# Kernel optimization log

Measured on AMD Instinct MI355X. Metric: run time of the kernel, lower is better.

The kernel has to match this reference:

```python
import jax, jax.numpy as jnp
import numpy as np

B, E, H, W = 32, 512, 16, 16
NH, HD = 8, 64          # num_heads = embed_dim // num_heads_channels, head_dim = 64
OUT = 512
S = H * W + 1           # spacial_dim**2 + 1 = 257 (mean token prepended)


def setup_inputs() -> dict:
    key = jax.random.key(0)
    ks = jax.random.split(key, 10)
    sc = 1.0 / np.sqrt(E).astype(np.float32)
    n = lambda k, sh, s=1.0: jax.random.normal(k, sh, jnp.float32) * s
    return {
        "x_real": n(ks[0], (B, E, H, W)),
        "x_imag": n(ks[1], (B, E, H, W)),
        # positional_embedding = (randn/sqrt(E)).to(complex64) -> imag part is zero
        "pos_r": n(ks[2], (E, S), sc),
        "pos_i": jnp.zeros((E, S), jnp.float32),
        # complex in-projection (packed q,k,v) and out-projection of the MHA
        "w_in_r": n(ks[3], (3 * E, E), sc),
        "w_in_i": n(ks[4], (3 * E, E), sc),
        "b_in_r": jnp.zeros((3 * E,), jnp.float32),
        "b_in_i": jnp.zeros((3 * E,), jnp.float32),
        "w_out_r": n(ks[5], (E, E), sc),
        "w_out_i": n(ks[6], (E, E), sc),
        "b_out_r": jnp.zeros((E,), jnp.float32),
        "b_out_i": jnp.zeros((E,), jnp.float32),
        # complex 1x1 conv projection == complex linear over channels
        "w_p_r": n(ks[7], (OUT, E), sc),
        "w_p_i": n(ks[8], (OUT, E), sc),
        "b_p_r": jnp.zeros((OUT,), jnp.float32),
        "b_p_i": jnp.zeros((OUT,), jnp.float32),
    }


def _attention_pool(x_real, x_imag, pos_r, pos_i, w_in_r, w_in_i, b_in_r, b_in_i,
                    w_out_r, w_out_i, b_out_r, b_out_i, w_p_r, w_p_i, b_p_r, b_p_i):
    cx = jax.lax.complex
    x = cx(x_real, x_imag).reshape(B, E, -1)                       # [b,c,HW]
    x = jnp.concatenate([x.mean(-1, keepdims=True), x], axis=-1)   # [b,c,S]
    x = x + cx(pos_r, pos_i)[None]                                 # + pos embed
    x = x.transpose(0, 2, 1)                                       # [b,S,E]

    qkv = jnp.einsum('bse,fe->bsf', x, cx(w_in_r, w_in_i)) + cx(b_in_r, b_in_i)
    q, k, v = jnp.split(qkv, 3, axis=-1)
    q = q.reshape(B, S, NH, HD) / jnp.sqrt(jnp.float32(HD))
    k = k.reshape(B, S, NH, HD)
    v = v.reshape(B, S, NH, HD)

    logits = jnp.einsum('bqhd,bkhd->bhqk', q, k)                   # complex scores
    # complex softmax handled separately on real/imag parts
    w = cx(jax.nn.softmax(logits.real, axis=-1),
           jax.nn.softmax(logits.imag, axis=-1))
    attn = jnp.einsum('bhqk,bkhd->bqhd', w, v).reshape(B, S, E)
    attn = jnp.einsum('bse,fe->bsf', attn, cx(w_out_r, w_out_i)) + cx(b_out_r, b_out_i)

    y = attn.transpose(0, 2, 1)                                    # [b,E,S]
    y = jnp.einsum('oc,bcs->bos', cx(w_p_r, w_p_i), y) + cx(b_p_r, b_p_i)[None, :, None]
    return y[:, :, 0]                                              # [b,OUT] complex64


def reference(x_real, x_imag, pos_r, pos_i, w_in_r, w_in_i, b_in_r, b_in_i,
              w_out_r, w_out_i, b_out_r, b_out_i, w_p_r, w_p_i, b_p_r, b_p_i):
    return _attention_pool(x_real, x_imag, pos_r, pos_i, w_in_r, w_in_i, b_in_r,
                           b_in_i, w_out_r, w_out_i, b_out_r, b_out_i,
                           w_p_r, w_p_i, b_p_r, b_p_i)
```

## Files before the change

### kernel.cpp

```cpp
#include <hip/hip_runtime.h>

#define B_   32
#define E_   512
#define HW_  256
#define S_   257
#define NH_  8
#define NBLK 1024
#define NTHR 256
#define NGRP 32
#define GSZ  32
#define LG_  260

__device__ __forceinline__ void st_sys(float* p, float v) {
  __hip_atomic_store(p, v, __ATOMIC_RELAXED, __HIP_MEMORY_SCOPE_SYSTEM);
}
__device__ __forceinline__ void st_sys2(float2* p, float2 v) {
  unsigned long long u;
  __builtin_memcpy(&u, &v, 8);
  __hip_atomic_store((unsigned long long*)p, u, __ATOMIC_RELAXED, __HIP_MEMORY_SCOPE_SYSTEM);
}

__device__ __forceinline__ float wave_reduce(float v) {
  #pragma unroll
  for (int o = 32; o > 0; o >>= 1) v += __shfl_down(v, o, 64);
  return v;
}

__device__ __forceinline__ void gbar(unsigned* slots, int g, int j, int t, unsigned phase) {
  __syncthreads();
  if (t < 64) {
    if (t == 0)
      __hip_atomic_store(&slots[g * GSZ + j], phase, __ATOMIC_RELAXED, __HIP_MEMORY_SCOPE_SYSTEM);
    const unsigned* line = slots + g * GSZ;
    int sl = t & 31;
    for (;;) {
      unsigned v = __hip_atomic_load(&line[sl], __ATOMIC_RELAXED, __HIP_MEMORY_SCOPE_SYSTEM);
      if (__all((int)(v >= phase))) break;
      __builtin_amdgcn_s_sleep(8);
    }
  }
  __syncthreads();
}

__device__ void softmax257(float* l, float* red, int t) {
  int lane = t & 63, wv = t >> 6;
  float v = l[t];
  float v256 = l[256];
  float m = v;
  #pragma unroll
  for (int o = 32; o > 0; o >>= 1) m = fmaxf(m, __shfl_xor(m, o, 64));
  if (lane == 0) red[wv] = m;
  __syncthreads();
  float M = fmaxf(fmaxf(fmaxf(red[0], red[1]), fmaxf(red[2], red[3])), v256);
  float ex = expf(v - M);
  float e256 = expf(v256 - M);
  float s = ex;
  #pragma unroll
  for (int o = 32; o > 0; o >>= 1) s += __shfl_xor(s, o, 64);
  if (lane == 0) red[4 + wv] = s;
  __syncthreads();
  float inv = 1.f / (red[4] + red[5] + red[6] + red[7] + e256);
  l[t] = ex * inv;
  if (t == 0) l[256] = e256 * inv;
  __syncthreads();
}

__global__ __launch_bounds__(NTHR, 4) void k_mega(
    const float* __restrict__ xr, const float* __restrict__ xi,
    const float* __restrict__ pos_r, const float* __restrict__ pos_i,
    const float* __restrict__ w_in_r, const float* __restrict__ w_in_i,
    const float* __restrict__ b_in_r, const float* __restrict__ b_in_i,
    const float* __restrict__ w_out_r, const float* __restrict__ w_out_i,
    const float* __restrict__ b_out_r, const float* __restrict__ b_out_i,
    const float* __restrict__ w_p_r, const float* __restrict__ w_p_i,
    const float* __restrict__ b_p_r, const float* __restrict__ b_p_i,
    unsigned* slots,
    float* __restrict__ ur_, float* __restrict__ ui_,
    float* __restrict__ lgr, float* __restrict__ lgi,
    float* __restrict__ a0r, float* __restrict__ a0i,
    float* __restrict__ mr, float* __restrict__ mi,
    float* __restrict__ w2,
    float* __restrict__ out, int interleaved) {
  __shared__ __align__(16) float smF[4368];
  const int t   = threadIdx.x;
  const int l   = t & 63;
  const int w   = t >> 6;
  const int bid = blockIdx.x;
  const int g   = bid >> 5;
  const int j   = bid & 31;

  #pragma unroll
  for (int rr = 0; rr < 4; ++rr) {
    int e = j * 16 + w * 4 + rr;
    float4 vr = ((const float4*)(xr + ((size_t)g * E_ + e) * HW_))[l];
    float4 vi = ((const float4*)(xi + ((size_t)g * E_ + e) * HW_))[l];
    float sr = (vr.x + vr.y) + (vr.z + vr.w);
    float si = (vi.x + vi.y) + (vi.z + vi.w);
    sr = wave_reduce(sr); si = wave_reduce(si);
    if (l == 0) {
      st_sys(&mr[g * E_ + e], sr * (1.f / HW_) + pos_r[(size_t)e * S_]);
      st_sys(&mi[g * E_ + e], si * (1.f / HW_) + pos_i[(size_t)e * S_]);
    }
  }
  gbar(slots, g, j, t, 1);

  {
    float* mR  = smF;
    float* mI  = smF + 512;
    float* q0L = smF + 1024;
    mR[t]       = mr[g * E_ + t];        mI[t]       = mi[g * E_ + t];
    mR[t + 256] = mr[g * E_ + t + 256];  mI[t + 256] = mi[g * E_ + t + 256];
    __syncthreads();
    #pragma unroll
    for (int rr = 0; rr < 4; ++rr) {
      int fl = w * 4 + rr;
      int f  = 16 * j + fl;
      const float* wr = w_in_r + (size_t)f * E_;
      const float* wi = w_in_i + (size_t)f * E_;
      float ar = 0.f, ai = 0.f;
      #pragma unroll
      for (int e = l; e < E_; e += 64) {
        float Xr = mR[e], Xi = mI[e], Cr = wr[e], Ci = wi[e];
        ar += Xr * Cr - Xi * Ci;
        ai += Xr * Ci + Xi * Cr;
      }
      ar = wave_reduce(ar); ai = wave_reduce(ai);
      if (l == 0) {
        q0L[fl * 2]     = (ar + b_in_r[f]) * 0.125f;
        q0L[fl * 2 + 1] = (ai + b_in_i[f]) * 0.125f;
      }
    }
    __syncthreads();
    int h = j >> 2;
    float u0r = 0.f, u0i = 0.f, u1r = 0.f, u1i = 0.f;
    #pragma unroll 4
    for (int fl = 0; fl < 16; ++fl) {
      int f = 16 * j + fl;
      float qr = q0L[fl * 2], qi = q0L[fl * 2 + 1];
      const float* Wr = w_in_r + (size_t)(E_ + f) * E_;
      const float* Wi = w_in_i + (size_t)(E_ + f) * E_;
      float W0r = Wr[t], W0i = Wi[t], W1r = Wr[t + 256], W1i = Wi[t + 256];
      u0r += qr * W0r - qi * W0i;  u0i += qr * W0i + qi * W0r;
      u1r += qr * W1r - qi * W1i;  u1i += qr * W1i + qi * W1r;
    }
    size_t ub = (size_t)(g * NH_ + h) * E_;
    atomicAdd(&ur_[ub + t], u0r);        atomicAdd(&ui_[ub + t], u0i);
    atomicAdd(&ur_[ub + t + 256], u1r);  atomicAdd(&ui_[ub + t + 256], u1i);
  }
  gbar(slots, g, j, t, 2);

  {
    int e0 = 16 * j;
    float* us = smF;
    if (t < 128) {
      int e = t & 15, hh = t >> 4;
      us[(e * 8 + hh) * 2]     = ur_[(size_t)(g * NH_ + hh) * E_ + e0 + e];
      us[(e * 8 + hh) * 2 + 1] = ui_[(size_t)(g * NH_ + hh) * E_ + e0 + e];
    }
    __syncthreads();
    float ar[NH_], ai[NH_];
    #pragma unroll
    for (int hh = 0; hh < NH_; ++hh) { ar[hh] = 0.f; ai[hh] = 0.f; }
    const float* xrb = xr + ((size_t)g * E_ + e0) * HW_;
    const float* xib = xi + ((size_t)g * E_ + e0) * HW_;
    #pragma unroll 2
    for (int e = 0; e < 16; ++e) {
      float Xr = xrb[e * HW_ + t] + pos_r[(size_t)(e0 + e) * S_ + t + 1];
      float Xi = xib[e * HW_ + t] + pos_i[(size_t)(e0 + e) * S_ + t + 1];
      #pragma unroll
      for (int hh = 0; hh < NH_; ++hh) {
        float Ur = us[(e * 8 + hh) * 2], Ui = us[(e * 8 + hh) * 2 + 1];
        ar[hh] += Xr * Ur - Xi * Ui;
        ai[hh] += Xr * Ui + Xi * Ur;
      }
    }
    #pragma unroll
    for (int hh = 0; hh < NH_; ++hh) {
      size_t lb = (size_t)(g * NH_ + hh) * LG_ + t + 1;
      atomicAdd(&lgr[lb], ar[hh]);
      atomicAdd(&lgi[lb], ai[hh]);
    }
  }
  gbar(slots, g, j, t, 3);

  if (j < NH_) {
    int bh = g * NH_ + j;
    float* lr  = smF;
    float* li  = smF + 260;
    float* redl = smF + 520;
    float* reds = smF + 528;
    lr[t + 1] = lgr[(size_t)bh * LG_ + t + 1];
    li[t + 1] = lgi[(size_t)bh * LG_ + t + 1];
    float pr = 0.f, pi = 0.f;
    #pragma unroll
    for (int e = t; e < E_; e += 256) {
      float Xr = mr[g * E_ + e], Xi = mi[g * E_ + e];
      float Ur = ur_[(size_t)bh * E_ + e], Ui = ui_[(size_t)bh * E_ + e];
      pr += Xr * Ur - Xi * Ui;
      pi += Xr * Ui + Xi * Ur;
    }
    pr = wave_reduce(pr); pi = wave_reduce(pi);
    if (l == 0) { redl[w * 2] = pr; redl[w * 2 + 1] = pi; }
    __syncthreads();
    if (t == 0) {
      lr[0] = redl[0] + redl[2] + redl[4] + redl[6];
      li[0] = redl[1] + redl[3] + redl[5] + redl[7];
    }
    __syncthreads();
    softmax257(lr, reds, t);
    softmax257(li, reds, t);
    float2* o = (float2*)w2 + (size_t)bh * S_;
    float2 v; v.x = lr[t]; v.y = li[t];
    st_sys2(&o[t], v);
    if (t == 0) { float2 v2; v2.x = lr[256]; v2.y = li[256]; st_sys2(&o[256], v2); }
  } else {
    int idx = t & 127;
    int e = 16 * j + (idx & 15);
    const float* src = (t < 128) ? xr : xi;
    float pf = src[((size_t)g * E_ + e) * HW_ + (idx >> 4) * 32];
    asm volatile("" :: "v"(pf));
  }
  gbar(slots, g, j, t, 4);

  {
    float2* wls = (float2*)smF;
    float*  zS  = smF + 4112;
    const float2* w2b = (const float2*)w2 + (size_t)g * NH_ * S_;
    for (int i = t; i < NH_ * S_; i += NTHR) wls[i] = w2b[i];
    __syncthreads();
    #pragma unroll
    for (int rr = 0; rr < 4; ++rr) {
      int el = 4 * w + rr;
      int e  = 16 * j + el;
      const float* xre = xr + ((size_t)g * E_ + e) * HW_;
      const float* xie = xi + ((size_t)g * E_ + e) * HW_;
      const float* pre = pos_r + (size_t)e * S_;
      const float* pie = pos_i + (size_t)e * S_;
      float ar2[NH_], ai2[NH_];
      #pragma unroll
      for (int hh = 0; hh < NH_; ++hh) { ar2[hh] = 0.f; ai2[hh] = 0.f; }
      #pragma unroll
      for (int jj = 0; jj < 4; ++jj) {
        int k = 1 + l + 64 * jj;
        float Xr = xre[k - 1] + pre[k];
        float Xi = xie[k - 1] + pie[k];
        #pragma unroll
        for (int hh = 0; hh < NH_; ++hh) {
          float2 W = wls[hh * S_ + k];
          ar2[hh] += W.x * Xr - W.y * Xi;
          ai2[hh] += W.x * Xi + W.y * Xr;
        }
      }
      #pragma unroll
      for (int hh = 0; hh < NH_; ++hh) { ar2[hh] = wave_reduce(ar2[hh]); ai2[hh] = wave_reduce(ai2[hh]); }
      if (l == 0) {
        float X0r = mr[g * E_ + e];
        float X0i = mi[g * E_ + e];
        #pragma unroll
        for (int hh = 0; hh < NH_; ++hh) {
          float2 W0 = wls[hh * S_];
          zS[(hh * 16 + el) * 2]     = ar2[hh] + W0.x * X0r - W0.y * X0i;
          zS[(hh * 16 + el) * 2 + 1] = ai2[hh] + W0.x * X0i + W0.y * X0r;
        }
      }
    }
    __syncthreads();
    #pragma unroll
    for (int ff = 0; ff < 2; ++ff) {
      int f  = t + ff * 256;
      int hh = f >> 6;
      const float* wvr = w_in_r + (size_t)(2 * E_ + f) * E_ + 16 * j;
      const float* wvi = w_in_i + (size_t)(2 * E_ + f) * E_ + 16 * j;
      float cr = 0.f, ci = 0.f;
      #pragma unroll
      for (int el = 0; el < 16; ++el) {
        float Wr = wvr[el], Wi = wvi[el];
        float Zr = zS[(hh * 16 + el) * 2], Zi = zS[(hh * 16 + el) * 2 + 1];
        cr += Wr * Zr - Wi * Zi;
        ci += Wr * Zi + Wi * Zr;
      }
      if (j == 0) {
        float bvr = b_in_r[2 * E_ + f], bvi = b_in_i[2 * E_ + f];
        cr += bvr - bvi;
        ci += bvr + bvi;
      }
      atomicAdd(&a0r[g * E_ + f], cr);
      atomicAdd(&a0i[g * E_ + f], ci);
    }
  }
  gbar(slots, g, j, t, 5);

  {
    float* aoS = smF;
    float* a0R = smF + 64;
    float* a0I = smF + 576;
    a0R[t]       = a0r[g * E_ + t];        a0I[t]       = a0i[g * E_ + t];
    a0R[t + 256] = a0r[g * E_ + t + 256];  a0I[t + 256] = a0i[g * E_ + t + 256];
    __syncthreads();
    #pragma unroll
    for (int rr = 0; rr < 4; ++rr) {
      int fl = w * 4 + rr;
      int f  = 16 * j + fl;
      const float* wrp = w_out_r + (size_t)f * E_;
      const float* wip = w_out_i + (size_t)f * E_;
      float ar = 0.f, ai = 0.f;
      #pragma unroll
      for (int e = l; e < E_; e += 64) {
        float Xr = a0R[e], Xi = a0I[e], Cr = wrp[e], Ci = wip[e];
        ar += Xr * Cr - Xi * Ci;
        ai += Xr * Ci + Xi * Cr;
      }
      ar = wave_reduce(ar); ai = wave_reduce(ai);
      if (l == 0) { aoS[fl * 2] = ar + b_out_r[f]; aoS[fl * 2 + 1] = ai + b_out_i[f]; }
    }
    __syncthreads();
    #pragma unroll
    for (int ff = 0; ff < 2; ++ff) {
      int o = t + ff * 256;
      const float* wpr = w_p_r + (size_t)o * E_ + 16 * j;
      const float* wpi = w_p_i + (size_t)o * E_ + 16 * j;
      float cr = 0.f, ci = 0.f;
      #pragma unroll
      for (int fl = 0; fl < 16; ++fl) {
        float Ar = aoS[fl * 2], Ai = aoS[fl * 2 + 1];
        float Wr = wpr[fl],     Wi = wpi[fl];
        cr += Ar * Wr - Ai * Wi;
        ci += Ar * Wi + Ai * Wr;
      }
      if (j == 0) { cr += b_p_r[o]; ci += b_p_i[o]; }
      int wid = g * E_ + o;
      if (interleaved) {
        atomicAdd(&out[(size_t)wid * 2],     cr);
        atomicAdd(&out[(size_t)wid * 2 + 1], ci);
      } else {
        atomicAdd(&out[wid], cr);
      }
    }
  }
}

extern "C" void kernel_launch(void* const* d_in, const int* in_sizes, int n_in,
                              void* d_out, int out_size, void* d_ws, size_t ws_size,
                              hipStream_t stream) {
  (void)in_sizes; (void)n_in; (void)ws_size;
  const float* xr      = (const float*)d_in[0];
  const float* xi      = (const float*)d_in[1];
  const float* pos_r   = (const float*)d_in[2];
  const float* pos_i   = (const float*)d_in[3];
  const float* w_in_r  = (const float*)d_in[4];
  const float* w_in_i  = (const float*)d_in[5];
  const float* b_in_r  = (const float*)d_in[6];
  const float* b_in_i  = (const float*)d_in[7];
  const float* w_out_r = (const float*)d_in[8];
  const float* w_out_i = (const float*)d_in[9];
  const float* b_out_r = (const float*)d_in[10];
  const float* b_out_i = (const float*)d_in[11];
  const float* w_p_r   = (const float*)d_in[12];
  const float* w_p_i   = (const float*)d_in[13];
  const float* b_p_r   = (const float*)d_in[14];
  const float* b_p_i   = (const float*)d_in[15];

  const int BE = B_ * E_, BHE = B_ * NH_ * E_;
  float* ws = (float*)d_ws;
  unsigned* slots = (unsigned*)d_ws;
  float* ur   = ws + 1024;
  float* ui   = ur + BHE;
  float* lgr  = ui + BHE;
  float* lgi  = lgr + B_ * NH_ * LG_;
  float* a0r  = lgi + B_ * NH_ * LG_;
  float* a0i  = a0r + BE;
  float* mr   = a0i + BE;
  float* mi   = mr + BE;
  float* w2   = mi + BE;

  int interleaved = out_size >= 2 * B_ * E_;

  size_t zbytes = (size_t)(1024 + 2 * BHE + 2 * B_ * NH_ * LG_ + 2 * BE) * 4;
  hipMemsetAsync(d_ws, 0, zbytes, stream);
  hipMemsetAsync(d_out, 0, (size_t)(interleaved ? 2 * BE : BE) * 4, stream);
  k_mega<<<NBLK, NTHR, 0, stream>>>(
      xr, xi, pos_r, pos_i, w_in_r, w_in_i, b_in_r, b_in_i,
      w_out_r, w_out_i, b_out_r, b_out_i, w_p_r, w_p_i, b_p_r, b_p_i,
      slots, ur, ui, lgr, lgi, a0r, a0i, mr, mi, w2,
      (float*)d_out, interleaved);
}
```

Before: 196.8 us.

## Cut grid barriers by redistributing q0, u, and softmax work across blocks

The kernel restructures the megakernel so each block computes a partial q0 from its own 16 channels and atomically accumulates it. Every block then recomputes its 16-channel slice of u for all heads locally instead of atomically accumulating full u vectors. Each block also redundantly computes the softmax of all 8 heads instead of having 8 designated blocks publish weights. This removes two of the five group barriers and the mr/mi/w2/u global buffers. In exchange it adds redundant softmax work per block, more atomics on q0, and scattered strided loads of w_in rows.

```diff
diff --git a/kernel.cpp b/kernel.cpp
--- a/kernel.cpp
+++ b/kernel.cpp
@@ -11,14 +11,10 @@
 #define GSZ  32
 #define LG_  260
 
-__device__ __forceinline__ void st_sys(float* p, float v) {
-  __hip_atomic_store(p, v, __ATOMIC_RELAXED, __HIP_MEMORY_SCOPE_SYSTEM);
-}
-__device__ __forceinline__ void st_sys2(float2* p, float2 v) {
-  unsigned long long u;
-  __builtin_memcpy(&u, &v, 8);
-  __hip_atomic_store((unsigned long long*)p, u, __ATOMIC_RELAXED, __HIP_MEMORY_SCOPE_SYSTEM);
-}
+#define RES_M 4112
+#define ZS_   4144
+#define SCR_  4400
+#define SMSZ  4416
 
 __device__ __forceinline__ float wave_reduce(float v) {
   #pragma unroll
@@ -42,29 +38,6 @@
   __syncthreads();
 }
 
-__device__ void softmax257(float* l, float* red, int t) {
-  int lane = t & 63, wv = t >> 6;
-  float v = l[t];
-  float v256 = l[256];
-  float m = v;
-  #pragma unroll
-  for (int o = 32; o > 0; o >>= 1) m = fmaxf(m, __shfl_xor(m, o, 64));
-  if (lane == 0) red[wv] = m;
-  __syncthreads();
-  float M = fmaxf(fmaxf(fmaxf(red[0], red[1]), fmaxf(red[2], red[3])), v256);
-  float ex = expf(v - M);
-  float e256 = expf(v256 - M);
-  float s = ex;
-  #pragma unroll
-  for (int o = 32; o > 0; o >>= 1) s += __shfl_xor(s, o, 64);
-  if (lane == 0) red[4 + wv] = s;
-  __syncthreads();
-  float inv = 1.f / (red[4] + red[5] + red[6] + red[7] + e256);
-  l[t] = ex * inv;
-  if (t == 0) l[256] = e256 * inv;
-  __syncthreads();
-}
-
 __global__ __launch_bounds__(NTHR, 4) void k_mega(
     const float* __restrict__ xr, const float* __restrict__ xi,
     const float* __restrict__ pos_r, const float* __restrict__ pos_i,
@@ -75,89 +48,99 @@
     const float* __restrict__ w_p_r, const float* __restrict__ w_p_i,
     const float* __restrict__ b_p_r, const float* __restrict__ b_p_i,
     unsigned* slots,
-    float* __restrict__ ur_, float* __restrict__ ui_,
+    float* __restrict__ q0a,
+    float* __restrict__ l0r, float* __restrict__ l0i,
     float* __restrict__ lgr, float* __restrict__ lgi,
     float* __restrict__ a0r, float* __restrict__ a0i,
-    float* __restrict__ mr, float* __restrict__ mi,
-    float* __restrict__ w2,
     float* __restrict__ out, int interleaved) {
-  __shared__ __align__(16) float smF[4368];
+  __shared__ __align__(16) float smF[SMSZ];
   const int t   = threadIdx.x;
   const int l   = t & 63;
   const int w   = t >> 6;
   const int bid = blockIdx.x;
   const int g   = bid >> 5;
   const int j   = bid & 31;
+  const int e0  = 16 * j;
+  float* mS = smF + RES_M;
 
   #pragma unroll
   for (int rr = 0; rr < 4; ++rr) {
-    int e = j * 16 + w * 4 + rr;
+    int el = w * 4 + rr;
+    int e  = e0 + el;
     float4 vr = ((const float4*)(xr + ((size_t)g * E_ + e) * HW_))[l];
     float4 vi = ((const float4*)(xi + ((size_t)g * E_ + e) * HW_))[l];
     float sr = (vr.x + vr.y) + (vr.z + vr.w);
     float si = (vi.x + vi.y) + (vi.z + vi.w);
     sr = wave_reduce(sr); si = wave_reduce(si);
     if (l == 0) {
-      st_sys(&mr[g * E_ + e], sr * (1.f / HW_) + pos_r[(size_t)e * S_]);
-      st_sys(&mi[g * E_ + e], si * (1.f / HW_) + pos_i[(size_t)e * S_]);
-    }
+      mS[el * 2]     = sr * (1.f / HW_) + pos_r[(size_t)e * S_];
+      mS[el * 2 + 1] = si * (1.f / HW_) + pos_i[(size_t)e * S_];
+    }
+  }
+  __syncthreads();
+  #pragma unroll
+  for (int ff = 0; ff < 2; ++ff) {
+    int f = t + ff * 256;
+    const float* wr = w_in_r + (size_t)f * E_ + e0;
+    const float* wi = w_in_i + (size_t)f * E_ + e0;
+    float ar = 0.f, ai = 0.f;
+    #pragma unroll
+    for (int el = 0; el < 16; ++el) {
+      float Xr = mS[el * 2], Xi = mS[el * 2 + 1];
+      float Cr = wr[el], Ci = wi[el];
+      ar += Xr * Cr - Xi * Ci;
+      ai += Xr * Ci + Xi * Cr;
+    }
+    atomicAdd(&q0a[(size_t)g * 1024 + f * 2], ar);
+    atomicAdd(&q0a[(size_t)g * 1024 + f * 2 + 1], ai);
   }
   gbar(slots, g, j, t, 1);
 
   {
-    float* mR  = smF;
-    float* mI  = smF + 512;
-    float* q0L = smF + 1024;
-    mR[t]       = mr[g * E_ + t];        mI[t]       = mi[g * E_ + t];
-    mR[t + 256] = mr[g * E_ + t + 256];  mI[t + 256] = mi[g * E_ + t + 256];
-    __syncthreads();
-    #pragma unroll
-    for (int rr = 0; rr < 4; ++rr) {
-      int fl = w * 4 + rr;
-      int f  = 16 * j + fl;
-      const float* wr = w_in_r + (size_t)f * E_;
-      const float* wi = w_in_i + (size_t)f * E_;
+    float* q0s = smF;
+    float* us  = smF + 1024;
+    float* pu  = smF + 1280;
+    #pragma unroll
+    for (int ff = 0; ff < 2; ++ff) {
+      int f = t + ff * 256;
+      q0s[f * 2]     = (q0a[(size_t)g * 1024 + f * 2]     + b_in_r[f]) * 0.125f;
+      q0s[f * 2 + 1] = (q0a[(size_t)g * 1024 + f * 2 + 1] + b_in_i[f]) * 0.125f;
+    }
+    __syncthreads();
+    {
+      int el = t & 15, hh = (t >> 4) & 7, dh = t >> 7;
       float ar = 0.f, ai = 0.f;
-      #pragma unroll
-      for (int e = l; e < E_; e += 64) {
-        float Xr = mR[e], Xi = mI[e], Cr = wr[e], Ci = wi[e];
-        ar += Xr * Cr - Xi * Ci;
-        ai += Xr * Ci + Xi * Cr;
-      }
-      ar = wave_reduce(ar); ai = wave_reduce(ai);
-      if (l == 0) {
-        q0L[fl * 2]     = (ar + b_in_r[f]) * 0.125f;
-        q0L[fl * 2 + 1] = (ai + b_in_i[f]) * 0.125f;
-      }
-    }
-    __syncthreads();
-    int h = j >> 2;
-    float u0r = 0.f, u0i = 0.f, u1r = 0.f, u1i = 0.f;
-    #pragma unroll 4
-    for (int fl = 0; fl < 16; ++fl) {
-      int f = 16 * j + fl;
-      float qr = q0L[fl * 2], qi = q0L[fl * 2 + 1];
-      const float* Wr = w_in_r + (size_t)(E_ + f) * E_;
-      const float* Wi = w_in_i + (size_t)(E_ + f) * E_;
-      float W0r = Wr[t], W0i = Wi[t], W1r = Wr[t + 256], W1i = Wi[t + 256];
-      u0r += qr * W0r - qi * W0i;  u0i += qr * W0i + qi * W0r;
-      u1r += qr * W1r - qi * W1i;  u1i += qr * W1i + qi * W1r;
-    }
-    size_t ub = (size_t)(g * NH_ + h) * E_;
-    atomicAdd(&ur_[ub + t], u0r);        atomicAdd(&ui_[ub + t], u0i);
-    atomicAdd(&ur_[ub + t + 256], u1r);  atomicAdd(&ui_[ub + t + 256], u1i);
-  }
-  gbar(slots, g, j, t, 2);
-
-  {
-    int e0 = 16 * j;
-    float* us = smF;
+      #pragma unroll 8
+      for (int dd = 0; dd < 32; ++dd) {
+        int f = hh * 64 + dh * 32 + dd;
+        float qr = q0s[f * 2], qi = q0s[f * 2 + 1];
+        float Wr = w_in_r[(size_t)(E_ + f) * E_ + e0 + el];
+        float Wi = w_in_i[(size_t)(E_ + f) * E_ + e0 + el];
+        ar += qr * Wr - qi * Wi;
+        ai += qr * Wi + qi * Wr;
+      }
+      pu[(dh * 128 + el * 8 + hh) * 2]     = ar;
+      pu[(dh * 128 + el * 8 + hh) * 2 + 1] = ai;
+    }
+    __syncthreads();
     if (t < 128) {
-      int e = t & 15, hh = t >> 4;
-      us[(e * 8 + hh) * 2]     = ur_[(size_t)(g * NH_ + hh) * E_ + e0 + e];
-      us[(e * 8 + hh) * 2 + 1] = ui_[(size_t)(g * NH_ + hh) * E_ + e0 + e];
-    }
-    __syncthreads();
+      int idx = t;
+      us[idx * 2]     = pu[idx * 2]     + pu[(128 + idx) * 2];
+      us[idx * 2 + 1] = pu[idx * 2 + 1] + pu[(128 + idx) * 2 + 1];
+    }
+    __syncthreads();
+    if (t < NH_) {
+      float pr = 0.f, pi = 0.f;
+      #pragma unroll
+      for (int el = 0; el < 16; ++el) {
+        float Xr = mS[el * 2], Xi = mS[el * 2 + 1];
+        float Ur = us[(el * 8 + t) * 2], Ui = us[(el * 8 + t) * 2 + 1];
+        pr += Xr * Ur - Xi * Ui;
+        pi += Xr * Ui + Xi * Ur;
+      }
+      atomicAdd(&l0r[g * NH_ + t], pr);
+      atomicAdd(&l0i[g * NH_ + t], pi);
+    }
     float ar[NH_], ai[NH_];
     #pragma unroll
     for (int hh = 0; hh < NH_; ++hh) { ar[hh] = 0.f; ai[hh] = 0.f; }
@@ -181,57 +164,55 @@
       atomicAdd(&lgi[lb], ai[hh]);
     }
   }
-  gbar(slots, g, j, t, 3);
-
-  if (j < NH_) {
-    int bh = g * NH_ + j;
-    float* lr  = smF;
-    float* li  = smF + 260;
-    float* redl = smF + 520;
-    float* reds = smF + 528;
-    lr[t + 1] = lgr[(size_t)bh * LG_ + t + 1];
-    li[t + 1] = lgi[(size_t)bh * LG_ + t + 1];
-    float pr = 0.f, pi = 0.f;
-    #pragma unroll
-    for (int e = t; e < E_; e += 256) {
-      float Xr = mr[g * E_ + e], Xi = mi[g * E_ + e];
-      float Ur = ur_[(size_t)bh * E_ + e], Ui = ui_[(size_t)bh * E_ + e];
-      pr += Xr * Ur - Xi * Ui;
-      pi += Xr * Ui + Xi * Ur;
-    }
-    pr = wave_reduce(pr); pi = wave_reduce(pi);
-    if (l == 0) { redl[w * 2] = pr; redl[w * 2 + 1] = pi; }
-    __syncthreads();
-    if (t == 0) {
-      lr[0] = redl[0] + redl[2] + redl[4] + redl[6];
-      li[0] = redl[1] + redl[3] + redl[5] + redl[7];
-    }
-    __syncthreads();
-    softmax257(lr, reds, t);
-    softmax257(li, reds, t);
-    float2* o = (float2*)w2 + (size_t)bh * S_;
-    float2 v; v.x = lr[t]; v.y = li[t];
-    st_sys2(&o[t], v);
-    if (t == 0) { float2 v2; v2.x = lr[256]; v2.y = li[256]; st_sys2(&o[256], v2); }
-  } else {
-    int idx = t & 127;
-    int e = 16 * j + (idx & 15);
-    const float* src = (t < 128) ? xr : xi;
-    float pf = src[((size_t)g * E_ + e) * HW_ + (idx >> 4) * 32];
-    asm volatile("" :: "v"(pf));
-  }
-  gbar(slots, g, j, t, 4);
+  gbar(slots, g, j, t, 2);
 
   {
     float2* wls = (float2*)smF;
-    float*  zS  = smF + 4112;
-    const float2* w2b = (const float2*)w2 + (size_t)g * NH_ * S_;
-    for (int i = t; i < NH_ * S_; i += NTHR) wls[i] = w2b[i];
-    __syncthreads();
+    float*  zS  = smF + ZS_;
+    float*  scr = smF + SCR_;
+    for (int i = t; i < NH_ * S_; i += NTHR) {
+      int hh = i / S_, k = i - hh * S_;
+      float2 v;
+      if (k == 0) { v.x = l0r[g * NH_ + hh];               v.y = l0i[g * NH_ + hh]; }
+      else        { v.x = lgr[(size_t)(g * NH_ + hh) * LG_ + k];
+                    v.y = lgi[(size_t)(g * NH_ + hh) * LG_ + k]; }
+      wls[i] = v;
+    }
+    __syncthreads();
+    for (int hh = 0; hh < NH_; ++hh) {
+      float2 v    = wls[hh * S_ + t];
+      float2 v256 = wls[hh * S_ + 256];
+      float mr_ = v.x, mi_ = v.y;
+      #pragma unroll
+      for (int o = 32; o > 0; o >>= 1) {
+        mr_ = fmaxf(mr_, __shfl_xor(mr_, o, 64));
+        mi_ = fmaxf(mi_, __shfl_xor(mi_, o, 64));
+      }
+      if (l == 0) { scr[w * 2] = mr_; scr[w * 2 + 1] = mi_; }
+      __syncthreads();
+      float Mr = fmaxf(fmaxf(fmaxf(scr[0], scr[2]), fmaxf(scr[4], scr[6])), v256.x);
+      float Mi = fmaxf(fmaxf(fmaxf(scr[1], scr[3]), fmaxf(scr[5], scr[7])), v256.y);
+      float exr = expf(v.x - Mr), exi = expf(v.y - Mi);
+      float e256r = expf(v256.x - Mr), e256i = expf(v256.y - Mi);
+      float sr_ = exr, si_ = exi;
+      #pragma unroll
+      for (int o = 32; o > 0; o >>= 1) {
+        sr_ += __shfl_xor(sr_, o, 64);
+        si_ += __shfl_xor(si_, o, 64);
+      }
+      if (l == 0) { scr[8 + w * 2] = sr_; scr[9 + w * 2] = si_; }
+      __syncthreads();
+      float invr = 1.f / (scr[8] + scr[10] + scr[12] + scr[14] + e256r);
+      float invi = 1.f / (scr[9] + scr[11] + scr[13] + scr[15] + e256i);
+      float2 wv; wv.x = exr * invr; wv.y = exi * invi;
+      wls[hh * S_ + t] = wv;
+      if (t == 0) { float2 w2v; w2v.x = e256r * invr; w2v.y = e256i * invi; wls[hh * S_ + 256] = w2v; }
+      __syncthreads();
+    }
     #pragma unroll
     for (int rr = 0; rr < 4; ++rr) {
       int el = 4 * w + rr;
-      int e  = 16 * j + el;
+      int e  = e0 + el;
       const float* xre = xr + ((size_t)g * E_ + e) * HW_;
       const float* xie = xi + ((size_t)g * E_ + e) * HW_;
       const float* pre = pos_r + (size_t)e * S_;
@@ -254,8 +235,8 @@
       #pragma unroll
       for (int hh = 0; hh < NH_; ++hh) { ar2[hh] = wave_reduce(ar2[hh]); ai2[hh] = wave_reduce(ai2[hh]); }
       if (l == 0) {
-        float X0r = mr[g * E_ + e];
-        float X0i = mi[g * E_ + e];
+        float X0r = mS[el * 2];
+        float X0i = mS[el * 2 + 1];
         #pragma unroll
         for (int hh = 0; hh < NH_; ++hh) {
           float2 W0 = wls[hh * S_];
@@ -269,8 +250,8 @@
     for (int ff = 0; ff < 2; ++ff) {
       int f  = t + ff * 256;
       int hh = f >> 6;
-      const float* wvr = w_in_r + (size_t)(2 * E_ + f) * E_ + 16 * j;
-      const float* wvi = w_in_i + (size_t)(2 * E_ + f) * E_ + 16 * j;
+      const float* wvr = w_in_r + (size_t)(2 * E_ + f) * E_ + e0;
+      const float* wvi = w_in_i + (size_t)(2 * E_ + f) * E_ + e0;
       float cr = 0.f, ci = 0.f;
       #pragma unroll
       for (int el = 0; el < 16; ++el) {
@@ -288,7 +269,7 @@
       atomicAdd(&a0i[g * E_ + f], ci);
     }
   }
-  gbar(slots, g, j, t, 5);
+  gbar(slots, g, j, t, 3);
 
   {
     float* aoS = smF;
@@ -360,27 +341,25 @@
   const float* b_p_r   = (const float*)d_in[14];
   const float* b_p_i   = (const float*)d_in[15];
 
-  const int BE = B_ * E_, BHE = B_ * NH_ * E_;
+  const int BE = B_ * E_;
   float* ws = (float*)d_ws;
   unsigned* slots = (unsigned*)d_ws;
-  float* ur   = ws + 1024;
-  float* ui   = ur + BHE;
-  float* lgr  = ui + BHE;
+  float* q0a  = ws + 1024;
+  float* l0r  = q0a + 32768;
+  float* l0i  = l0r + 256;
+  float* lgr  = l0i + 256;
   float* lgi  = lgr + B_ * NH_ * LG_;
   float* a0r  = lgi + B_ * NH_ * LG_;
   float* a0i  = a0r + BE;
-  float* mr   = a0i + BE;
-  float* mi   = mr + BE;
-  float* w2   = mi + BE;
 
   int interleaved = out_size >= 2 * B_ * E_;
 
-  size_t zbytes = (size_t)(1024 + 2 * BHE + 2 * B_ * NH_ * LG_ + 2 * BE) * 4;
+  size_t zbytes = (size_t)(1024 + 32768 + 512 + 2 * B_ * NH_ * LG_ + 2 * BE) * 4;
   hipMemsetAsync(d_ws, 0, zbytes, stream);
   hipMemsetAsync(d_out, 0, (size_t)(interleaved ? 2 * BE : BE) * 4, stream);
   k_mega<<<NBLK, NTHR, 0, stream>>>(
       xr, xi, pos_r, pos_i, w_in_r, w_in_i, b_in_r, b_in_i,
       w_out_r, w_out_i, b_out_r, b_out_i, w_p_r, w_p_i, b_p_r, b_p_i,
-      slots, ur, ui, lgr, lgi, a0r, a0i, mr, mi, w2,
+      slots, q0a, l0r, l0i, lgr, lgi, a0r, a0i,
       (float*)d_out, interleaved);
 }
```

Result: slower. 211.6 us (+7.5%).
